# Performance work log

Hardware: AMD Instinct MI355X
Metric: run time of the kernel (lower is better)

Reference implementation:

```python
import jax, jax.numpy as jnp
import numpy as np


def _mlp(x, w1, b1, w2, b2):
    # full_connected / full_connected_conv1d with channels [3,16,32]:
    # pointwise Linear -> LeakyReLU -> Linear (kernel-size-1 conv == linear on last dim)
    h = jax.nn.leaky_relu(x @ w1 + b1)
    return h @ w2 + b2


def setup_inputs() -> dict:
    key = jax.random.key(0)
    ks = jax.random.split(key, 10)
    P, K = 100000, 16            # points, neighbors per point
    C_IN, C_H, C_OUT, C_W = 3, 16, 32, 64
    center = jax.random.normal(ks[0], (P, 1, C_IN), dtype=jnp.float32)
    other = jax.random.normal(ks[1], (P, K, C_IN), dtype=jnp.float32)
    s1 = 1.0 / np.sqrt(C_IN)
    s2 = 1.0 / np.sqrt(C_H)
    # 6 stacked 3->16->32 MLPs: [q, center_k, center_v, other_k, other_v, pos]
    mlp_w1 = jax.random.normal(ks[2], (6, C_IN, C_H), dtype=jnp.float32) * s1
    mlp_b1 = jax.random.normal(ks[3], (6, C_H), dtype=jnp.float32) * s1
    mlp_w2 = jax.random.normal(ks[4], (6, C_H, C_OUT), dtype=jnp.float32) * s2
    mlp_b2 = jax.random.normal(ks[5], (6, C_OUT), dtype=jnp.float32) * s2
    # weight_process: 32->64->32
    wp_w1 = jax.random.normal(ks[6], (C_OUT, C_W), dtype=jnp.float32) / np.sqrt(C_OUT)
    wp_b1 = jax.random.normal(ks[7], (C_W,), dtype=jnp.float32) / np.sqrt(C_OUT)
    wp_w2 = jax.random.normal(ks[8], (C_W, C_OUT), dtype=jnp.float32) / np.sqrt(C_W)
    wp_b2 = jax.random.normal(ks[9], (C_OUT,), dtype=jnp.float32) / np.sqrt(C_W)
    return {"center": center, "other": other,
            "mlp_w1": mlp_w1, "mlp_b1": mlp_b1, "mlp_w2": mlp_w2, "mlp_b2": mlp_b2,
            "wp_w1": wp_w1, "wp_b1": wp_b1, "wp_w2": wp_w2, "wp_b2": wp_b2}


def reference(center, other, mlp_w1, mlp_b1, mlp_w2, mlp_b2, wp_w1, wp_b1, wp_w2, wp_b2):
    # center: [P,1,3], other: [P,K,3]
    q = _mlp(center, mlp_w1[0], mlp_b1[0], mlp_w2[0], mlp_b2[0])      # [P,1,32]
    ck = _mlp(center, mlp_w1[1], mlp_b1[1], mlp_w2[1], mlp_b2[1])     # [P,1,32]
    cv = _mlp(center, mlp_w1[2], mlp_b1[2], mlp_w2[2], mlp_b2[2])     # [P,1,32]
    ok = _mlp(other, mlp_w1[3], mlp_b1[3], mlp_w2[3], mlp_b2[3])      # [P,K,32]
    ov = _mlp(other, mlp_w1[4], mlp_b1[4], mlp_w2[4], mlp_b2[4])      # [P,K,32]
    k_all = jnp.concatenate([ck, ok], axis=-2)                        # [P,K+1,32]
    v_all = jnp.concatenate([cv, ov], axis=-2)                        # [P,K+1,32]
    fea_minus = center - jnp.concatenate([center, other], axis=-2)    # [P,K+1,3]
    pos = _mlp(fea_minus, mlp_w1[5], mlp_b1[5], mlp_w2[5], mlp_b2[5]) # [P,K+1,32]
    fea_weight = _mlp(q - k_all + pos, wp_w1, wp_b1, wp_w2, wp_b2)    # [P,K+1,32]
    # vector attention: softmax over CHANNEL dim (-1), weighted sum over neighbors (-2)
    attn = jax.nn.softmax(fea_weight, axis=-1) * (v_all + pos)
    return jnp.sum(attn, axis=-2)                                     # [P,32]
```

## Files before the change

kernel.cpp:

```cpp
#include <hip/hip_runtime.h>
#include <hip/hip_bf16.h>


constexpr int PPB = 15;

typedef __attribute__((ext_vector_type(8))) short bf8;
typedef __attribute__((ext_vector_type(4))) short bf4;
typedef __attribute__((ext_vector_type(4))) float f4;

__device__ __forceinline__ float lrelu(float v) { return v > 0.f ? v : 0.01f * v; }

__device__ __forceinline__ unsigned int pkbf(float a, float b) {
  const unsigned int ua = __builtin_bit_cast(unsigned int, a) + 0x8000u;
  const unsigned int ub = __builtin_bit_cast(unsigned int, b) + 0x8000u;
  return __builtin_amdgcn_perm(ub, ua, 0x07060302u);
}
__device__ __forceinline__ bf4 mkbf4(float v0, float v1, float v2, float v3) {
  uint2 u; u.x = pkbf(v0, v1); u.y = pkbf(v2, v3);
  return __builtin_bit_cast(bf4, u);
}
__device__ __forceinline__ float bf2f_lo(unsigned int u) {
  return __builtin_bit_cast(float, u << 16);
}
__device__ __forceinline__ float bf2f_hi(unsigned int u) {
  return __builtin_bit_cast(float, u & 0xffff0000u);
}

__device__ __forceinline__ f4 mfma16(bf4 a, bf4 b, f4 c) {
#if __has_builtin(__builtin_amdgcn_mfma_f32_16x16x16_bf16)
  return __builtin_amdgcn_mfma_f32_16x16x16_bf16(a, b, c, 0, 0, 0);
#elif __has_builtin(__builtin_amdgcn_mfma_f32_16x16x16bf16_1k)
  return __builtin_amdgcn_mfma_f32_16x16x16bf16_1k(a, b, c, 0, 0, 0);
#else
  f4 d;
  asm volatile("v_mfma_f32_16x16x16_bf16 %0, %1, %2, %3"
               : "=&v"(d) : "v"(a), "v"(b), "v"(c));
  return d;
#endif
}

__device__ float w1v(const float* mw1, const float* mb1, int s, int k, int n) {
  const int cb = n >> 4, cc = n & 15;
  const int sk = s ? 1 : 3, sv = s ? 2 : 4;
  if (k < 3)  return cb == 0 ? mw1[sk * 48 + k * 16 + cc]
                   : (cb == 1 ? mw1[sv * 48 + k * 16 + cc] : 0.f);
  if (k < 6)  return cb == 2 ? mw1[5 * 48 + (k - 3) * 16 + cc] : 0.f;
  if (k < 9)  return cb == 3 ? mw1[0 * 48 + (k - 6) * 16 + cc] : 0.f;
  if (k == 9) {
    const int m = (cb == 0) ? sk : (cb == 1) ? sv : (cb == 2) ? 5 : 0;
    return mb1[m * 16 + cc];
  }
  return 0.f;
}
__device__ float w2v(const float* mw2, int s, int k, int n) {
  const int sk = s ? 1 : 3, sv = s ? 2 : 4;
  if (n < 32) {
    if (k < 16)            return -mw2[sk * 512 + k * 32 + n];
    if (k >= 32 && k < 48) return  mw2[5 * 512 + (k - 32) * 32 + n];
    if (k >= 48)           return  mw2[0 * 512 + (k - 48) * 32 + n];
    return 0.f;
  } else {
    const int cc = n - 32;
    if (k >= 16 && k < 32) return mw2[sv * 512 + (k - 16) * 32 + cc];
    if (k >= 32 && k < 48) return mw2[5 * 512 + (k - 32) * 32 + cc];
    return 0.f;
  }
}

__global__ void prep_kernel(const float* __restrict__ mw1, const float* __restrict__ mb1,
                            const float* __restrict__ mw2, const float* __restrict__ mb2,
                            const float* __restrict__ ww1, const float* __restrict__ ww2,
                            unsigned short* __restrict__ ws16, float* __restrict__ wsf) {
  const int tid = blockIdx.x * 256 + threadIdx.x;
  const int lane = tid & 63, q = lane >> 4, l = lane & 15;
  if (tid < 512) {
    const int f = tid >> 6, s = f >> 2, c = f & 3;
    for (int j = 0; j < 8; j++)
      ws16[f * 512 + lane * 8 + j] =
          (unsigned short)(pkbf(w1v(mw1, mb1, s, q * 8 + j, c * 16 + l), 0.f) & 0xffffu);
  } else if (tid < 2560) {
    const int f = (tid - 512) >> 6, s = f >> 4, mc = (f >> 2) & 3, kc = f & 3;
    for (int j = 0; j < 4; j++)
      ws16[4096 + f * 256 + lane * 4 + j] =
          (unsigned short)(pkbf(w2v(mw2, s, kc * 16 + q * 4 + j, mc * 16 + l), 0.f) & 0xffffu);
  } else if (tid < 3072) {
    const int f = (tid - 2560) >> 6, mc = f >> 1, kc = f & 1;
    for (int j = 0; j < 4; j++)
      ws16[12288 + f * 256 + lane * 4 + j] =
          (unsigned short)(pkbf(ww1[(kc * 16 + q * 4 + j) * 64 + mc * 16 + l], 0.f) & 0xffffu);
  } else if (tid < 3584) {
    const int f = (tid - 3072) >> 6, mc = f >> 2, kc = f & 3;
    for (int j = 0; j < 4; j++)
      ws16[14336 + f * 256 + lane * 4 + j] =
          (unsigned short)(pkbf(ww2[(kc * 16 + q * 4 + j) * 32 + mc * 16 + l], 0.f) & 0xffffu);
  } else if (tid < 3712) {
    const int t2 = tid - 3584, grp = t2 >> 5, cc = t2 & 31;
    float v;
    if (grp == 0)      v = mb2[cc] - mb2[96 + cc] + mb2[160 + cc];
    else if (grp == 1) v = mb2[128 + cc] + mb2[160 + cc];
    else if (grp == 2) v = mb2[cc] - mb2[32 + cc] + mb2[160 + cc];
    else               v = mb2[64 + cc] + mb2[160 + cc];
    wsf[grp * 32 + cc] = v;
  }
}

__global__ __launch_bounds__(256, 3) void point_attn_kernel(
    const float* __restrict__ center, const float* __restrict__ other,
    const float* __restrict__ wb1, const float* __restrict__ wb2,
    const unsigned short* __restrict__ ws16, const float* __restrict__ wsf,
    float* __restrict__ out, int P) {
  __shared__ float pr[256 * 36];

  const int t = threadIdx.x, lane = t & 63, wv = t >> 6;
  const int q = lane >> 4, l = lane & 15;
  const f4 fzero = {0.f, 0.f, 0.f, 0.f};

  unsigned int d0, d1, d2, d3, d4;
  {
    const int isC = (t >= 240);
    const int pt = isC ? (t - 240) : (t >> 4);
    int p = blockIdx.x * PPB + pt;
    p = p < P ? p : P - 1;
    const float c0 = center[(size_t)p * 3 + 0];
    const float c1 = center[(size_t)p * 3 + 1];
    const float c2 = center[(size_t)p * 3 + 2];
    const float* op = other + ((size_t)p * 16 + (t & 15)) * 3;
    const float o0 = op[0], o1 = op[1], o2 = op[2];
    const float x0 = isC ? c0 : o0, x1 = isC ? c1 : o1, x2 = isC ? c2 : o2;
    const float g0 = c0 - x0, g1 = c1 - x1, g2 = c2 - x2;
    d0 = pkbf(x0, x1); d1 = pkbf(x2, g0); d2 = pkbf(g1, g2);
    d3 = pkbf(c0, c1); d4 = pkbf(c2, 1.0f);
  }

  bf8 W1[4]; bf4 W2[4][4]; f4 bw[2], bvp[2];
  bf4 P1[4][2], P2[2][4];
  unsigned int bp1[4][2], bp2[2][2];

  auto loadSet = [&](int s) {
#pragma unroll
    for (int c = 0; c < 4; c++)
      W1[c] = *(const bf8*)(ws16 + ((s * 4 + c) * 64 + lane) * 8);
#pragma unroll
    for (int mc = 0; mc < 4; mc++)
#pragma unroll
      for (int kc = 0; kc < 4; kc++)
        W2[mc][kc] = *(const bf4*)(ws16 + 4096 + ((s * 16 + mc * 4 + kc) * 64 + lane) * 4);
#pragma unroll
    for (int mc = 0; mc < 2; mc++) {
      bw[mc]  = *(const f4*)(wsf + s * 64 + mc * 16 + q * 4);
      bvp[mc] = *(const f4*)(wsf + s * 64 + 32 + mc * 16 + q * 4);
    }
  };

  loadSet(wv == 3 ? 1 : 0);
#pragma unroll
  for (int mc = 0; mc < 4; mc++)
#pragma unroll
    for (int kc = 0; kc < 2; kc++)
      P1[mc][kc] = *(const bf4*)(ws16 + 12288 + ((mc * 2 + kc) * 64 + lane) * 4);
#pragma unroll
  for (int mc = 0; mc < 2; mc++)
#pragma unroll
    for (int kc = 0; kc < 4; kc++)
      P2[mc][kc] = *(const bf4*)(ws16 + 14336 + ((mc * 4 + kc) * 64 + lane) * 4);
#pragma unroll
  for (int mc = 0; mc < 4; mc++) {
    const f4 b = *(const f4*)(wb1 + mc * 16 + q * 4);
    bp1[mc][0] = pkbf(b[0], b[1]); bp1[mc][1] = pkbf(b[2], b[3]);
  }
#pragma unroll
  for (int mc = 0; mc < 2; mc++) {
    const f4 b = *(const f4*)(wb2 + mc * 16 + q * 4);
    bp2[mc][0] = pkbf(b[0], b[1]); bp2[mc][1] = pkbf(b[2], b[3]);
  }

  auto computeTile = [&](int T) {
    const int src = ((T & 3) << 4) | l;
    const unsigned int s0 = __shfl((int)d0, src), s1 = __shfl((int)d1, src),
                       s2 = __shfl((int)d2, src), s3 = __shfl((int)d3, src),
                       s4 = __shfl((int)d4, src);
    uint4 bu;
    bu.x = q == 0 ? s0 : (q == 1 ? s4 : 0u);
    bu.y = q == 0 ? s1 : 0u;
    bu.z = q == 0 ? s2 : 0u;
    bu.w = q == 0 ? s3 : 0u;
    const bf8 bx = __builtin_bit_cast(bf8, bu);

    bf4 hB[4];
#pragma unroll
    for (int c = 0; c < 4; c++) {
      const f4 D1 = __builtin_amdgcn_mfma_f32_16x16x32_bf16(W1[c], bx, fzero, 0, 0, 0);
      hB[c] = mkbf4(lrelu(D1[0]), lrelu(D1[1]), lrelu(D1[2]), lrelu(D1[3]));
    }

    bf4 wB[2]; float vpv[2][4];
#pragma unroll
    for (int mc = 0; mc < 4; mc++) {
      f4 acc = fzero;
#pragma unroll
      for (int kc = 0; kc < 4; kc++) acc = mfma16(W2[mc][kc], hB[kc], acc);
      if (mc < 2) {
        wB[mc] = mkbf4(acc[0] + bw[mc][0], acc[1] + bw[mc][1],
                       acc[2] + bw[mc][2], acc[3] + bw[mc][3]);
      } else {
#pragma unroll
        for (int j = 0; j < 4; j++) vpv[mc - 2][j] = acc[j] + bvp[mc - 2][j];
      }
    }

    bf4 h2B[4];
#pragma unroll
    for (int mc = 0; mc < 4; mc++) {
      f4 acc = fzero;
#pragma unroll
      for (int kc = 0; kc < 2; kc++) acc = mfma16(P1[mc][kc], wB[kc], acc);
      h2B[mc] = mkbf4(lrelu(acc[0] + bf2f_lo(bp1[mc][0])),
                      lrelu(acc[1] + bf2f_hi(bp1[mc][0])),
                      lrelu(acc[2] + bf2f_lo(bp1[mc][1])),
                      lrelu(acc[3] + bf2f_hi(bp1[mc][1])));
    }

    float fw[2][4];
#pragma unroll
    for (int mc = 0; mc < 2; mc++) {
      f4 acc = fzero;
#pragma unroll
      for (int kc = 0; kc < 4; kc++) acc = mfma16(P2[mc][kc], h2B[kc], acc);
      fw[mc][0] = acc[0] + bf2f_lo(bp2[mc][0]);
      fw[mc][1] = acc[1] + bf2f_hi(bp2[mc][0]);
      fw[mc][2] = acc[2] + bf2f_lo(bp2[mc][1]);
      fw[mc][3] = acc[3] + bf2f_hi(bp2[mc][1]);
    }

    float mx = fw[0][0];
#pragma unroll
    for (int mc = 0; mc < 2; mc++)
#pragma unroll
      for (int j = 0; j < 4; j++) mx = fmaxf(mx, fw[mc][j]);
    mx = fmaxf(mx, __shfl_xor(mx, 16));
    mx = fmaxf(mx, __shfl_xor(mx, 32));
    float e[2][4], sum = 0.f;
#pragma unroll
    for (int mc = 0; mc < 2; mc++)
#pragma unroll
      for (int j = 0; j < 4; j++) { e[mc][j] = __expf(fw[mc][j] - mx); sum += e[mc][j]; }
    sum += __shfl_xor(sum, 16);
    sum += __shfl_xor(sum, 32);
    const float inv = 1.f / sum;

    f4 p0, p1;
#pragma unroll
    for (int j = 0; j < 4; j++) {
      p0[j] = e[0][j] * inv * vpv[0][j];
      p1[j] = e[1][j] * inv * vpv[1][j];
    }
    *(f4*)&pr[(T * 16 + l) * 36 + q * 4] = p0;
    *(f4*)&pr[(T * 16 + l) * 36 + 16 + q * 4] = p1;
  };

  computeTile(wv == 3 ? 15 : wv * 4);
  if (wv == 3) loadSet(0);
  for (int jj = 1; jj < 4; jj++)
    computeTile(wv == 3 ? (11 + jj) : (wv * 4 + jj));

  __syncthreads();

  for (int u = t; u < 480; u += 256) {
    const int pp = u >> 5, c = u & 31;
    float s = pr[(240 + pp) * 36 + c];
#pragma unroll
    for (int r2 = 0; r2 < 16; r2++) s += pr[(pp * 16 + r2) * 36 + c];
    const int gp = blockIdx.x * PPB + pp;
    if (gp < P) out[(size_t)gp * 32 + c] = s;
  }
}

extern "C" void kernel_launch(void* const* d_in, const int* in_sizes, int n_in,
                              void* d_out, int out_size, void* d_ws, size_t ws_size,
                              hipStream_t stream) {
  const float* center = (const float*)d_in[0];
  const float* other  = (const float*)d_in[1];
  unsigned short* ws16 = (unsigned short*)d_ws;
  float* wsf = (float*)((char*)d_ws + 32768);

  prep_kernel<<<15, 256, 0, stream>>>(
      (const float*)d_in[2], (const float*)d_in[3],
      (const float*)d_in[4], (const float*)d_in[5],
      (const float*)d_in[6], (const float*)d_in[8], ws16, wsf);

  const int P = in_sizes[0] / 3;
  const int blocks = (P + PPB - 1) / PPB;
  point_attn_kernel<<<blocks, 256, 0, stream>>>(
      center, other,
      (const float*)d_in[7], (const float*)d_in[9],
      ws16, wsf, (float*)d_out, P);
}
```

Measured before the change: 155.2 us.

## Switch MLP chain to 16x16x32 MFMA with K-slot packed weights and fused biases

```diff
diff --git a/kernel.cpp b/kernel.cpp
--- a/kernel.cpp
+++ b/kernel.cpp
@@ -1,45 +1,44 @@
 #include <hip/hip_runtime.h>
-#include <hip/hip_bf16.h>
 
 
 constexpr int PPB = 15;
+constexpr float LOG2E = 1.44269504088896340736f;
 
 typedef __attribute__((ext_vector_type(8))) short bf8;
-typedef __attribute__((ext_vector_type(4))) short bf4;
 typedef __attribute__((ext_vector_type(4))) float f4;
 
-__device__ __forceinline__ float lrelu(float v) { return v > 0.f ? v : 0.01f * v; }
-
+__device__ __forceinline__ float lrelu(float v) { return fmaxf(v, 0.01f * v); }
 __device__ __forceinline__ unsigned int pkbf(float a, float b) {
   const unsigned int ua = __builtin_bit_cast(unsigned int, a) + 0x8000u;
   const unsigned int ub = __builtin_bit_cast(unsigned int, b) + 0x8000u;
   return __builtin_amdgcn_perm(ub, ua, 0x07060302u);
 }
-__device__ __forceinline__ bf4 mkbf4(float v0, float v1, float v2, float v3) {
-  uint2 u; u.x = pkbf(v0, v1); u.y = pkbf(v2, v3);
-  return __builtin_bit_cast(bf4, u);
-}
-__device__ __forceinline__ float bf2f_lo(unsigned int u) {
-  return __builtin_bit_cast(float, u << 16);
-}
-__device__ __forceinline__ float bf2f_hi(unsigned int u) {
-  return __builtin_bit_cast(float, u & 0xffff0000u);
-}
-
-__device__ __forceinline__ f4 mfma16(bf4 a, bf4 b, f4 c) {
-#if __has_builtin(__builtin_amdgcn_mfma_f32_16x16x16_bf16)
-  return __builtin_amdgcn_mfma_f32_16x16x16_bf16(a, b, c, 0, 0, 0);
-#elif __has_builtin(__builtin_amdgcn_mfma_f32_16x16x16bf16_1k)
-  return __builtin_amdgcn_mfma_f32_16x16x16bf16_1k(a, b, c, 0, 0, 0);
+__device__ __forceinline__ unsigned short us16(float a) {
+  return (unsigned short)((__builtin_bit_cast(unsigned int, a) + 0x8000u) >> 16);
+}
+__device__ __forceinline__ bf8 mkbf8(const f4& a, const f4& b) {
+  uint4 u;
+  u.x = pkbf(a[0], a[1]); u.y = pkbf(a[2], a[3]);
+  u.z = pkbf(b[0], b[1]); u.w = pkbf(b[2], b[3]);
+  return __builtin_bit_cast(bf8, u);
+}
+__device__ __forceinline__ float exp2fast(float x) {
+#if __has_builtin(__builtin_amdgcn_exp2f)
+  return __builtin_amdgcn_exp2f(x);
 #else
-  f4 d;
-  asm volatile("v_mfma_f32_16x16x16_bf16 %0, %1, %2, %3"
-               : "=&v"(d) : "v"(a), "v"(b), "v"(c));
-  return d;
+  float r; asm("v_exp_f32 %0, %1" : "=v"(r) : "v"(x)); return r;
 #endif
 }
-
-__device__ float w1v(const float* mw1, const float* mb1, int s, int k, int n) {
+__device__ __forceinline__ f4 mfma32(bf8 a, bf8 b, f4 c) {
+  return __builtin_amdgcn_mfma_f32_16x16x32_bf16(a, b, c, 0, 0, 0);
+}
+
+__device__ __forceinline__ int slotk(int q, int j) {
+  return (j < 4) ? (q * 4 + j) : (16 + q * 4 + (j - 4));
+}
+
+__device__ __forceinline__ float w1v(const float* mw1, const float* mb1,
+                                     int s, int k, int n) {
   const int cb = n >> 4, cc = n & 15;
   const int sk = s ? 1 : 3, sv = s ? 2 : 4;
   if (k < 3)  return cb == 0 ? mw1[sk * 48 + k * 16 + cc]
@@ -52,7 +51,7 @@
   }
   return 0.f;
 }
-__device__ float w2v(const float* mw2, int s, int k, int n) {
+__device__ __forceinline__ float w2v(const float* mw2, int s, int k, int n) {
   const int sk = s ? 1 : 3, sv = s ? 2 : 4;
   if (n < 32) {
     if (k < 16)            return -mw2[sk * 512 + k * 32 + n];
@@ -73,28 +72,27 @@
                             unsigned short* __restrict__ ws16, float* __restrict__ wsf) {
   const int tid = blockIdx.x * 256 + threadIdx.x;
   const int lane = tid & 63, q = lane >> 4, l = lane & 15;
-  if (tid < 512) {
-    const int f = tid >> 6, s = f >> 2, c = f & 3;
-    for (int j = 0; j < 8; j++)
-      ws16[f * 512 + lane * 8 + j] =
-          (unsigned short)(pkbf(w1v(mw1, mb1, s, q * 8 + j, c * 16 + l), 0.f) & 0xffffu);
-  } else if (tid < 2560) {
-    const int f = (tid - 512) >> 6, s = f >> 4, mc = (f >> 2) & 3, kc = f & 3;
-    for (int j = 0; j < 4; j++)
-      ws16[4096 + f * 256 + lane * 4 + j] =
-          (unsigned short)(pkbf(w2v(mw2, s, kc * 16 + q * 4 + j, mc * 16 + l), 0.f) & 0xffffu);
-  } else if (tid < 3072) {
-    const int f = (tid - 2560) >> 6, mc = f >> 1, kc = f & 1;
-    for (int j = 0; j < 4; j++)
-      ws16[12288 + f * 256 + lane * 4 + j] =
-          (unsigned short)(pkbf(ww1[(kc * 16 + q * 4 + j) * 64 + mc * 16 + l], 0.f) & 0xffffu);
-  } else if (tid < 3584) {
-    const int f = (tid - 3072) >> 6, mc = f >> 2, kc = f & 3;
-    for (int j = 0; j < 4; j++)
-      ws16[14336 + f * 256 + lane * 4 + j] =
-          (unsigned short)(pkbf(ww2[(kc * 16 + q * 4 + j) * 32 + mc * 16 + l], 0.f) & 0xffffu);
-  } else if (tid < 3712) {
-    const int t2 = tid - 3584, grp = t2 >> 5, cc = t2 & 31;
+  if (tid < 2048) {
+    const int f = tid >> 6;
+    for (int j = 0; j < 8; j++) {
+      float v;
+      if (f < 8) {
+        const int s = f >> 2, c = f & 3;
+        v = w1v(mw1, mb1, s, q * 8 + j, c * 16 + l);
+      } else if (f < 24) {
+        const int g = f - 8, s = g >> 3, mc = (g >> 1) & 3, kc2 = g & 1;
+        v = w2v(mw2, s, kc2 * 32 + slotk(q, j), mc * 16 + l);
+      } else if (f < 28) {
+        const int mc = f - 24;
+        v = ww1[slotk(q, j) * 64 + mc * 16 + l];
+      } else {
+        const int g = f - 28, mc2 = g >> 1, kc2 = g & 1;
+        v = ww2[(kc2 * 32 + slotk(q, j)) * 32 + mc2 * 16 + l] * LOG2E;
+      }
+      ws16[f * 512 + lane * 8 + j] = us16(v);
+    }
+  } else if (tid < 2176) {
+    const int t2 = tid - 2048, grp = t2 >> 5, cc = t2 & 31;
     float v;
     if (grp == 0)      v = mb2[cc] - mb2[96 + cc] + mb2[160 + cc];
     else if (grp == 1) v = mb2[128 + cc] + mb2[160 + cc];
@@ -113,7 +111,6 @@
 
   const int t = threadIdx.x, lane = t & 63, wv = t >> 6;
   const int q = lane >> 4, l = lane & 15;
-  const f4 fzero = {0.f, 0.f, 0.f, 0.f};
 
   unsigned int d0, d1, d2, d3, d4;
   {
@@ -132,19 +129,18 @@
     d3 = pkbf(c0, c1); d4 = pkbf(c2, 1.0f);
   }
 
-  bf8 W1[4]; bf4 W2[4][4]; f4 bw[2], bvp[2];
-  bf4 P1[4][2], P2[2][4];
-  unsigned int bp1[4][2], bp2[2][2];
+  bf8 W1[4], W2[4][2], P1[4], P2[2][2];
+  f4 bw[2], bvp[2], b1f[4], b2f[2];
 
   auto loadSet = [&](int s) {
 #pragma unroll
     for (int c = 0; c < 4; c++)
-      W1[c] = *(const bf8*)(ws16 + ((s * 4 + c) * 64 + lane) * 8);
+      W1[c] = *(const bf8*)(ws16 + ((s * 4 + c) * 512 + lane * 8));
 #pragma unroll
     for (int mc = 0; mc < 4; mc++)
 #pragma unroll
-      for (int kc = 0; kc < 4; kc++)
-        W2[mc][kc] = *(const bf4*)(ws16 + 4096 + ((s * 16 + mc * 4 + kc) * 64 + lane) * 4);
+      for (int kc2 = 0; kc2 < 2; kc2++)
+        W2[mc][kc2] = *(const bf8*)(ws16 + ((8 + s * 8 + mc * 2 + kc2) * 512 + lane * 8));
 #pragma unroll
     for (int mc = 0; mc < 2; mc++) {
       bw[mc]  = *(const f4*)(wsf + s * 64 + mc * 16 + q * 4);
@@ -155,23 +151,19 @@
   loadSet(wv == 3 ? 1 : 0);
 #pragma unroll
   for (int mc = 0; mc < 4; mc++)
-#pragma unroll
-    for (int kc = 0; kc < 2; kc++)
-      P1[mc][kc] = *(const bf4*)(ws16 + 12288 + ((mc * 2 + kc) * 64 + lane) * 4);
-#pragma unroll
-  for (int mc = 0; mc < 2; mc++)
-#pragma unroll
-    for (int kc = 0; kc < 4; kc++)
-      P2[mc][kc] = *(const bf4*)(ws16 + 14336 + ((mc * 4 + kc) * 64 + lane) * 4);
-#pragma unroll
-  for (int mc = 0; mc < 4; mc++) {
-    const f4 b = *(const f4*)(wb1 + mc * 16 + q * 4);
-    bp1[mc][0] = pkbf(b[0], b[1]); bp1[mc][1] = pkbf(b[2], b[3]);
-  }
-#pragma unroll
-  for (int mc = 0; mc < 2; mc++) {
-    const f4 b = *(const f4*)(wb2 + mc * 16 + q * 4);
-    bp2[mc][0] = pkbf(b[0], b[1]); bp2[mc][1] = pkbf(b[2], b[3]);
+    P1[mc] = *(const bf8*)(ws16 + ((24 + mc) * 512 + lane * 8));
+#pragma unroll
+  for (int mc2 = 0; mc2 < 2; mc2++)
+#pragma unroll
+    for (int kc2 = 0; kc2 < 2; kc2++)
+      P2[mc2][kc2] = *(const bf8*)(ws16 + ((28 + mc2 * 2 + kc2) * 512 + lane * 8));
+#pragma unroll
+  for (int mc = 0; mc < 4; mc++) b1f[mc] = *(const f4*)(wb1 + mc * 16 + q * 4);
+#pragma unroll
+  for (int mc2 = 0; mc2 < 2; mc2++) {
+    const f4 b = *(const f4*)(wb2 + mc2 * 16 + q * 4);
+#pragma unroll
+    for (int j = 0; j < 4; j++) b2f[mc2][j] = b[j] * LOG2E;
   }
 
   auto computeTile = [&](int T) {
@@ -185,51 +177,43 @@
     bu.z = q == 0 ? s2 : 0u;
     bu.w = q == 0 ? s3 : 0u;
     const bf8 bx = __builtin_bit_cast(bf8, bu);
-
-    bf4 hB[4];
+    const f4 fzero = {0.f, 0.f, 0.f, 0.f};
+
+    f4 D1[4];
 #pragma unroll
     for (int c = 0; c < 4; c++) {
-      const f4 D1 = __builtin_amdgcn_mfma_f32_16x16x32_bf16(W1[c], bx, fzero, 0, 0, 0);
-      hB[c] = mkbf4(lrelu(D1[0]), lrelu(D1[1]), lrelu(D1[2]), lrelu(D1[3]));
-    }
-
-    bf4 wB[2]; float vpv[2][4];
+      f4 D = mfma32(W1[c], bx, fzero);
+#pragma unroll
+      for (int j = 0; j < 4; j++) D1[c][j] = lrelu(D[j]);
+    }
+    const bf8 hlo = mkbf8(D1[0], D1[1]);
+    const bf8 hhi = mkbf8(D1[2], D1[3]);
+
+    f4 wq[2], vpv[2];
 #pragma unroll
     for (int mc = 0; mc < 4; mc++) {
-      f4 acc = fzero;
-#pragma unroll
-      for (int kc = 0; kc < 4; kc++) acc = mfma16(W2[mc][kc], hB[kc], acc);
-      if (mc < 2) {
-        wB[mc] = mkbf4(acc[0] + bw[mc][0], acc[1] + bw[mc][1],
-                       acc[2] + bw[mc][2], acc[3] + bw[mc][3]);
-      } else {
-#pragma unroll
-        for (int j = 0; j < 4; j++) vpv[mc - 2][j] = acc[j] + bvp[mc - 2][j];
-      }
-    }
-
-    bf4 h2B[4];
+      f4 acc = (mc < 2) ? bw[mc] : bvp[mc - 2];
+      acc = mfma32(W2[mc][0], hlo, acc);
+      acc = mfma32(W2[mc][1], hhi, acc);
+      if (mc < 2) wq[mc] = acc; else vpv[mc - 2] = acc;
+    }
+    const bf8 wB = mkbf8(wq[0], wq[1]);
+
+    f4 h2[4];
 #pragma unroll
     for (int mc = 0; mc < 4; mc++) {
-      f4 acc = fzero;
-#pragma unroll
-      for (int kc = 0; kc < 2; kc++) acc = mfma16(P1[mc][kc], wB[kc], acc);
-      h2B[mc] = mkbf4(lrelu(acc[0] + bf2f_lo(bp1[mc][0])),
-                      lrelu(acc[1] + bf2f_hi(bp1[mc][0])),
-                      lrelu(acc[2] + bf2f_lo(bp1[mc][1])),
-                      lrelu(acc[3] + bf2f_hi(bp1[mc][1])));
-    }
-
-    float fw[2][4];
-#pragma unroll
-    for (int mc = 0; mc < 2; mc++) {
-      f4 acc = fzero;
-#pragma unroll
-      for (int kc = 0; kc < 4; kc++) acc = mfma16(P2[mc][kc], h2B[kc], acc);
-      fw[mc][0] = acc[0] + bf2f_lo(bp2[mc][0]);
-      fw[mc][1] = acc[1] + bf2f_hi(bp2[mc][0]);
-      fw[mc][2] = acc[2] + bf2f_lo(bp2[mc][1]);
-      fw[mc][3] = acc[3] + bf2f_hi(bp2[mc][1]);
+      f4 acc = mfma32(P1[mc], wB, b1f[mc]);
+#pragma unroll
+      for (int j = 0; j < 4; j++) h2[mc][j] = lrelu(acc[j]);
+    }
+    const bf8 h2lo = mkbf8(h2[0], h2[1]);
+    const bf8 h2hi = mkbf8(h2[2], h2[3]);
+
+    f4 fw[2];
+#pragma unroll
+    for (int mc2 = 0; mc2 < 2; mc2++) {
+      f4 acc = mfma32(P2[mc2][0], h2lo, b2f[mc2]);
+      fw[mc2] = mfma32(P2[mc2][1], h2hi, acc);
     }
 
     float mx = fw[0][0];
@@ -239,20 +223,23 @@
       for (int j = 0; j < 4; j++) mx = fmaxf(mx, fw[mc][j]);
     mx = fmaxf(mx, __shfl_xor(mx, 16));
     mx = fmaxf(mx, __shfl_xor(mx, 32));
-    float e[2][4], sum = 0.f;
+    float ex[2][4], sum = 0.f;
 #pragma unroll
     for (int mc = 0; mc < 2; mc++)
 #pragma unroll
-      for (int j = 0; j < 4; j++) { e[mc][j] = __expf(fw[mc][j] - mx); sum += e[mc][j]; }
+      for (int j = 0; j < 4; j++) {
+        ex[mc][j] = exp2fast(fw[mc][j] - mx);
+        sum += ex[mc][j];
+      }
     sum += __shfl_xor(sum, 16);
     sum += __shfl_xor(sum, 32);
-    const float inv = 1.f / sum;
+    const float inv = __builtin_amdgcn_rcpf(sum);
 
     f4 p0, p1;
 #pragma unroll
     for (int j = 0; j < 4; j++) {
-      p0[j] = e[0][j] * inv * vpv[0][j];
-      p1[j] = e[1][j] * inv * vpv[1][j];
+      p0[j] = ex[0][j] * inv * vpv[0][j];
+      p1[j] = ex[1][j] * inv * vpv[1][j];
     }
     *(f4*)&pr[(T * 16 + l) * 36 + q * 4] = p0;
     *(f4*)&pr[(T * 16 + l) * 36 + 16 + q * 4] = p1;
@@ -283,7 +270,7 @@
   unsigned short* ws16 = (unsigned short*)d_ws;
   float* wsf = (float*)((char*)d_ws + 32768);
 
-  prep_kernel<<<15, 256, 0, stream>>>(
+  prep_kernel<<<9, 256, 0, stream>>>(
       (const float*)d_in[2], (const float*)d_in[3],
       (const float*)d_in[4], (const float*)d_in[5],
       (const float*)d_in[6], (const float*)d_in[8], ws16, wsf);
```

Result: faster. 145.9 us (-6.0%).
